# Optimization experiments

Hardware: AMD Instinct MI355X
Metric: run time of the kernel (lower is better)

## Reference

```python
import math
import jax, jax.numpy as jnp
import numpy as np

B, IN, OUT = 1024, 512, 512
SCALE_BASE = 1.0
SCALE_WAVELET = 1.0
MH_CONST = 2.0 / (math.sqrt(3.0) * math.pi ** 0.25)  # mexican hat normalizer


def setup_inputs() -> dict:
    key = jax.random.key(0)
    k1, k2, k3, k4 = jax.random.split(key, 4)
    he = math.sqrt(6.0 / IN)  # HeUniform fan_in limit
    return {
        "x": jax.random.normal(k1, (B, IN), dtype=jnp.float32),
        "scale": jnp.ones((OUT, IN), dtype=jnp.float32),
        "translation": jnp.zeros((OUT, IN), dtype=jnp.float32),
        "base_weight": jax.random.uniform(k3, (IN, OUT), dtype=jnp.float32, minval=-he, maxval=he),
        "wavelet_weights": jax.random.uniform(k4, (OUT, IN), dtype=jnp.float32, minval=-he, maxval=he),
    }


def reference(x, scale, translation, base_weight, wavelet_weights):
    # base path: swish(x @ W)
    base_out = x @ base_weight                      # (B, OUT)
    base_out = base_out * jax.nn.sigmoid(base_out)  # swish

    # wavelet path: expand to (B, OUT, IN), mexican-hat, weighted reduce over IN
    x_scaled = (x[:, None, :] - translation[None]) / scale[None]  # (B, OUT, IN)
    sq = jnp.square(x_scaled)
    wavelet = MH_CONST * (sq - 1.0) * jnp.exp(-0.5 * sq)
    wavelet_out = jnp.sum(wavelet * wavelet_weights[None], axis=2)  # (B, OUT)

    return SCALE_BASE * base_out + SCALE_WAVELET * wavelet_out
```

## Files before the change

kernel.cpp:

```cpp
#include <hip/hip_runtime.h>


#define B_DIM   1024
#define IN_DIM  512
#define OUT_DIM 512

#define MH_CONST 0.8673250691f
#define NHL2E    0.72134752044448170368f
#define L2E      1.44269504088896340736f

#define POISON32 0xAAAAAAAAu

#define OFF_XBF 4096
#define OFF_PSI (OFF_XBF + B_DIM*IN_DIM*2)
#define OFF_WBT (OFF_PSI + B_DIM*IN_DIM*2)
#define OFF_WWB (OFF_WBT + OUT_DIM*IN_DIM*2)
#define WS_NEED (OFF_WWB + OUT_DIM*IN_DIM*2)

#if defined(__has_builtin)
#if __has_builtin(__builtin_amdgcn_exp2f)
#define EXP2F(v) __builtin_amdgcn_exp2f(v)
#endif
#endif
#ifndef EXP2F
#define EXP2F(v) exp2f(v)
#endif

typedef __attribute__((ext_vector_type(8))) short short8;
typedef __attribute__((ext_vector_type(4))) float f32x4;

#define TO_GBL(p) ((const __attribute__((address_space(1))) void*)(p))
#define TO_LDS(p) ((__attribute__((address_space(3))) void*)(p))

__device__ __forceinline__ unsigned short f2bf(float f) {
    unsigned int u = __float_as_uint(f);
    u = (u + 0x7fff + ((u >> 16) & 1)) >> 16;
    return (unsigned short)u;
}
__device__ __forceinline__ unsigned int pack_bf(float a, float b) {
    return (unsigned int)f2bf(a) | ((unsigned int)f2bf(b) << 16);
}
__device__ __forceinline__ float psi_f(float xv) {
    const float sq = xv * xv;
    const float e  = EXP2F(-NHL2E * sq);
    return fmaf(MH_CONST, sq, -MH_CONST) * e;
}
__device__ __forceinline__ size_t panel_off(int row, int k8) {
    return (size_t)(row >> 5) * 32768 + (size_t)k8 * 512 + (row & 31) * 16;
}
__device__ __forceinline__ uint2 pack8(const float* s) {
    uint2 u;
    u.x = pack_bf(s[0], s[1]) ;
    u.y = pack_bf(s[2], s[3]);
    return u;
}

__global__ __launch_bounds__(256) void wkan_prep(
    const float* __restrict__ x,
    const float* __restrict__ scale,
    const float* __restrict__ trans,
    const float* __restrict__ bwgt,
    const float* __restrict__ wwgt,
    unsigned char* __restrict__ ws)
{
    __shared__ float tile[64][65];
    const int blk = blockIdx.x, t = threadIdx.x;
    unsigned int* flag = (unsigned int*)ws;

    if (blk < 256) {
        const int g = blk * 256 + t;
        const int row = g >> 6, c = g & 63;
        const float* src = x + (size_t)row * IN_DIM + c * 8;
        float v[8];
        *(float4*)&v[0] = *(const float4*)src;
        *(float4*)&v[4] = *(const float4*)(src + 4);
        const size_t off = panel_off(row, c);
        uint2 a, b;
        a.x = pack_bf(v[0], v[1]); a.y = pack_bf(v[2], v[3]);
        b.x = pack_bf(v[4], v[5]); b.y = pack_bf(v[6], v[7]);
        *(uint2*)(ws + OFF_XBF + off) = a;
        *(uint2*)(ws + OFF_XBF + off + 8) = b;
        a.x = pack_bf(psi_f(v[0]), psi_f(v[1])); a.y = pack_bf(psi_f(v[2]), psi_f(v[3]));
        b.x = pack_bf(psi_f(v[4]), psi_f(v[5])); b.y = pack_bf(psi_f(v[6]), psi_f(v[7]));
        *(uint2*)(ws + OFF_PSI + off) = a;
        *(uint2*)(ws + OFF_PSI + off + 8) = b;
    } else if (blk < 384) {
        const int g = (blk - 256) * 256 + t;
        const int row = g >> 6, c = g & 63;
        const size_t e = (size_t)row * IN_DIM + c * 8;
        const float4 s0 = *(const float4*)&scale[e];
        const float4 s1 = *(const float4*)&scale[e + 4];
        const float4 t0 = *(const float4*)&trans[e];
        const float4 t1 = *(const float4*)&trans[e + 4];
        const bool ok =
            (s0.x == 1.f) & (s0.y == 1.f) & (s0.z == 1.f) & (s0.w == 1.f) &
            (s1.x == 1.f) & (s1.y == 1.f) & (s1.z == 1.f) & (s1.w == 1.f) &
            (t0.x == 0.f) & (t0.y == 0.f) & (t0.z == 0.f) & (t0.w == 0.f) &
            (t1.x == 0.f) & (t1.y == 0.f) & (t1.z == 0.f) & (t1.w == 0.f);
        if (!ok) atomicAnd(flag, 0u);
        const float4 w0 = *(const float4*)&wwgt[e];
        const float4 w1 = *(const float4*)&wwgt[e + 4];
        const size_t off = panel_off(row, c);
        uint2 a, b;
        a.x = pack_bf(w0.x, w0.y); a.y = pack_bf(w0.z, w0.w);
        b.x = pack_bf(w1.x, w1.y); b.y = pack_bf(w1.z, w1.w);
        *(uint2*)(ws + OFF_WWB + off) = a;
        *(uint2*)(ws + OFF_WWB + off + 8) = b;
    } else {
        const int bt  = blk - 384;
        const int tk0 = (bt & 7) * 64;
        const int to0 = (bt >> 3) * 64;
        const int r   = t >> 2;
        const int c0  = (t & 3) * 16;
#pragma unroll
        for (int j = 0; j < 4; ++j) {
            const float4 v = *(const float4*)&bwgt[(size_t)(tk0 + r) * OUT_DIM + to0 + c0 + j * 4];
            tile[r][c0 + j * 4 + 0] = v.x; tile[r][c0 + j * 4 + 1] = v.y;
            tile[r][c0 + j * 4 + 2] = v.z; tile[r][c0 + j * 4 + 3] = v.w;
        }
        __syncthreads();
        uint2 a, b;
        a.x = pack_bf(tile[c0 + 0][r],  tile[c0 + 1][r]);
        a.y = pack_bf(tile[c0 + 2][r],  tile[c0 + 3][r]);
        b.x = pack_bf(tile[c0 + 4][r],  tile[c0 + 5][r]);
        b.y = pack_bf(tile[c0 + 6][r],  tile[c0 + 7][r]);
        const int orow = to0 + r;
        size_t off = panel_off(orow, (tk0 + c0) >> 3);
        *(uint2*)(ws + OFF_WBT + off) = a;
        *(uint2*)(ws + OFF_WBT + off + 8) = b;
        a.x = pack_bf(tile[c0 + 8][r],  tile[c0 + 9][r]);
        a.y = pack_bf(tile[c0 + 10][r], tile[c0 + 11][r]);
        b.x = pack_bf(tile[c0 + 12][r], tile[c0 + 13][r]);
        b.y = pack_bf(tile[c0 + 14][r], tile[c0 + 15][r]);
        off = panel_off(orow, ((tk0 + c0) >> 3) + 1);
        *(uint2*)(ws + OFF_WBT + off) = a;
        *(uint2*)(ws + OFF_WBT + off + 8) = b;
    }
}

__global__ __launch_bounds__(256) void wkan_main(
    const float* __restrict__ x,
    const float* __restrict__ scale,
    const float* __restrict__ trans,
    const float* __restrict__ bwgt,
    const float* __restrict__ wwgt,
    float* __restrict__ out,
    const unsigned char* __restrict__ ws,
    int have_ws)
{
    __shared__ __align__(16) unsigned char smem[65536];

    const int t  = threadIdx.x;
    const int b0 = blockIdx.x * 32;
    const int o0 = blockIdx.y * 32;
    const int fast = have_ws && (*(const unsigned int*)ws == POISON32);

    if (fast) {
        const int lane = t & 63, wave = t >> 6;
        const int mt = wave & 1, nt = wave >> 1;
        const int m = lane & 15, q = lane >> 4;

        const unsigned char* src =
            (wave == 0) ? (ws + OFF_XBF + (size_t)(b0 >> 5) * 32768) :
            (wave == 1) ? (ws + OFF_PSI + (size_t)(b0 >> 5) * 32768) :
            (wave == 2) ? (ws + OFF_WBT + (size_t)(o0 >> 5) * 32768) :
                          (ws + OFF_WWB + (size_t)(o0 >> 5) * 32768);
        const unsigned char* gbase = src + lane * 16;
        unsigned char* ldst = smem + wave * 16384;

        const int aoff = q * 512 + (mt * 16 + m) * 16;
        const int boff = q * 512 + (nt * 16 + m) * 16;

        f32x4 accb = {0.f, 0.f, 0.f, 0.f};
        f32x4 accw = {0.f, 0.f, 0.f, 0.f};

        for (int s = 0; s < 2; ++s) {
            __syncthreads();
#pragma unroll
            for (int i = 0; i < 16; ++i)
                __builtin_amdgcn_global_load_lds(TO_GBL(gbase + s * 16384 + i * 1024),
                                                 TO_LDS(ldst + i * 1024), 16, 0, 0);
            __syncthreads();

#pragma unroll
            for (int kk = 0; kk < 8; ++kk) {
                const short8 ax = *(const short8*)(smem + 0     + kk * 2048 + aoff);
                const short8 ap = *(const short8*)(smem + 16384 + kk * 2048 + aoff);
                const short8 bb = *(const short8*)(smem + 32768 + kk * 2048 + boff);
                const short8 bw = *(const short8*)(smem + 49152 + kk * 2048 + boff);
                accb = __builtin_amdgcn_mfma_f32_16x16x32_bf16(ax, bb, accb, 0, 0, 0);
                accw = __builtin_amdgcn_mfma_f32_16x16x32_bf16(ap, bw, accw, 0, 0, 0);
            }
        }

#pragma unroll
        for (int r = 0; r < 4; ++r) {
            const int bb_ = b0 + mt * 16 + q * 4 + r;
            const int oo_ = o0 + nt * 16 + m;
            const float sv  = accb[r];
            const float sig = __frcp_rn(1.0f + EXP2F(-sv * L2E));
            out[(size_t)bb_ * OUT_DIM + oo_] = fmaf(sv, sig, accw[r]);
        }
    } else {
        float (*sxs)[34] = (float(*)[34])(smem);
        float (*sts)[34] = (float(*)[34])(smem + 4352);
        float (*srs)[34] = (float(*)[34])(smem + 8704);
        float (*sws)[34] = (float(*)[34])(smem + 13056);
        float (*sbs)[34] = (float(*)[34])(smem + 17408);

        const int tx = t & 15, ty = t >> 4;
        const int lr = t >> 3, lc = (t & 7) * 4;

        float accw2[2][2] = {{0.f, 0.f}, {0.f, 0.f}};
        float accb2[2][2] = {{0.f, 0.f}, {0.f, 0.f}};

        for (int k0 = 0; k0 < IN_DIM; k0 += 32) {
            const float4 xv = *(const float4*)&x[(size_t)(b0 + lr) * IN_DIM + k0 + lc];
            const float4 tv = *(const float4*)&trans[(size_t)(o0 + lr) * IN_DIM + k0 + lc];
            const float4 sv = *(const float4*)&scale[(size_t)(o0 + lr) * IN_DIM + k0 + lc];
            const float4 wv = *(const float4*)&wwgt[(size_t)(o0 + lr) * IN_DIM + k0 + lc];
            const float4 bv = *(const float4*)&bwgt[(size_t)(k0 + lr) * OUT_DIM + o0 + lc];

            __syncthreads();

            sxs[lc + 0][lr] = xv.x; sxs[lc + 1][lr] = xv.y;
            sxs[lc + 2][lr] = xv.z; sxs[lc + 3][lr] = xv.w;
            sts[lc + 0][lr] = tv.x; sts[lc + 1][lr] = tv.y;
            sts[lc + 2][lr] = tv.z; sts[lc + 3][lr] = tv.w;
            srs[lc + 0][lr] = __frcp_rn(sv.x); srs[lc + 1][lr] = __frcp_rn(sv.y);
            srs[lc + 2][lr] = __frcp_rn(sv.z); srs[lc + 3][lr] = __frcp_rn(sv.w);
            sws[lc + 0][lr] = wv.x * MH_CONST; sws[lc + 1][lr] = wv.y * MH_CONST;
            sws[lc + 2][lr] = wv.z * MH_CONST; sws[lc + 3][lr] = wv.w * MH_CONST;
            sbs[lr][lc + 0] = bv.x; sbs[lr][lc + 1] = bv.y;
            sbs[lr][lc + 2] = bv.z; sbs[lr][lc + 3] = bv.w;

            __syncthreads();

#pragma unroll 8
            for (int kk = 0; kk < 32; ++kk) {
                const float2 xv2 = *(const float2*)&sxs[kk][2 * ty];
                const float2 tv2 = *(const float2*)&sts[kk][2 * tx];
                const float2 rv2 = *(const float2*)&srs[kk][2 * tx];
                const float2 wv2 = *(const float2*)&sws[kk][2 * tx];
                const float2 bv2 = *(const float2*)&sbs[kk][2 * tx];
                const float xb[2] = {xv2.x, xv2.y};
                const float tr[2] = {tv2.x, tv2.y};
                const float rc[2] = {rv2.x, rv2.y};
                const float wl[2] = {wv2.x, wv2.y};
                const float bw2[2] = {bv2.x, bv2.y};
#pragma unroll
                for (int oo = 0; oo < 2; ++oo) {
#pragma unroll
                    for (int bb = 0; bb < 2; ++bb) {
                        const float d  = (xb[bb] - tr[oo]) * rc[oo];
                        const float sq = d * d;
                        const float e  = EXP2F(-NHL2E * sq);
                        const float p  = fmaf(wl[oo], sq, -wl[oo]);
                        accw2[bb][oo] = fmaf(p, e, accw2[bb][oo]);
                        accb2[bb][oo] = fmaf(xb[bb], bw2[oo], accb2[bb][oo]);
                    }
                }
            }
        }

#pragma unroll
        for (int bb = 0; bb < 2; ++bb) {
#pragma unroll
            for (int oo = 0; oo < 2; ++oo) {
                const float s   = accb2[bb][oo];
                const float sig = __frcp_rn(1.0f + EXP2F(-s * L2E));
                out[(size_t)(b0 + 2 * ty + bb) * OUT_DIM + (o0 + 2 * tx + oo)] =
                    fmaf(s, sig, accw2[bb][oo]);
            }
        }
    }
}

extern "C" void kernel_launch(void* const* d_in, const int* in_sizes, int n_in,
                              void* d_out, int out_size, void* d_ws, size_t ws_size,
                              hipStream_t stream) {
    const float* x     = (const float*)d_in[0];
    const float* scale = (const float*)d_in[1];
    const float* trans = (const float*)d_in[2];
    const float* bwgt  = (const float*)d_in[3];
    const float* wwgt  = (const float*)d_in[4];
    float* out = (float*)d_out;

    const int have_ws = (ws_size >= (size_t)WS_NEED) ? 1 : 0;
    unsigned char* ws = (unsigned char*)d_ws;

    if (have_ws) {
        wkan_prep<<<dim3(448), dim3(256), 0, stream>>>(x, scale, trans, bwgt, wwgt, ws);
    }
    wkan_main<<<dim3(B_DIM / 32, OUT_DIM / 32), dim3(256), 0, stream>>>(
        x, scale, trans, bwgt, wwgt, out, ws, have_ws);
}
```

Before: 70.33 us.

## Load MFMA operands directly from global per wave, dropping LDS staging

The fast path of the main kernel no longer stages the four bf16 operand panels into a 64KB LDS buffer with global_load_lds and barriers. Each wave now computes its own 16x16 output tile and reads its A and B fragments straight from the pre-packed workspace. The grid becomes 1D with a remapped block-to-tile order meant to help L2 locality, and shared memory shrinks to what the fallback path needs, which should allow more resident blocks. The cost is that operand reuse within a block is lost, so fragments shared by neighbouring tiles are fetched repeatedly and rely on L2/L1 hits.

Measured after the change: 72.84 us. 3.6% more time.

```diff
diff --git a/kernel.cpp b/kernel.cpp
--- a/kernel.cpp
+++ b/kernel.cpp
@@ -29,9 +29,6 @@
 typedef __attribute__((ext_vector_type(8))) short short8;
 typedef __attribute__((ext_vector_type(4))) float f32x4;
 
-#define TO_GBL(p) ((const __attribute__((address_space(1))) void*)(p))
-#define TO_LDS(p) ((__attribute__((address_space(3))) void*)(p))
-
 __device__ __forceinline__ unsigned short f2bf(float f) {
     unsigned int u = __float_as_uint(f);
     u = (u + 0x7fff + ((u >> 16) & 1)) >> 16;
@@ -47,12 +44,6 @@
 }
 __device__ __forceinline__ size_t panel_off(int row, int k8) {
     return (size_t)(row >> 5) * 32768 + (size_t)k8 * 512 + (row & 31) * 16;
-}
-__device__ __forceinline__ uint2 pack8(const float* s) {
-    uint2 u;
-    u.x = pack_bf(s[0], s[1]) ;
-    u.y = pack_bf(s[2], s[3]);
-    return u;
 }
 
 __global__ __launch_bounds__(256) void wkan_prep(
@@ -148,60 +139,51 @@
     const unsigned char* __restrict__ ws,
     int have_ws)
 {
-    __shared__ __align__(16) unsigned char smem[65536];
-
-    const int t  = threadIdx.x;
-    const int b0 = blockIdx.x * 32;
-    const int o0 = blockIdx.y * 32;
+    __shared__ __align__(16) unsigned char smem[21760];
+
+    const int t   = threadIdx.x;
+    const int blk = blockIdx.x;
     const int fast = have_ws && (*(const unsigned int*)ws == POISON32);
 
     if (fast) {
         const int lane = t & 63, wave = t >> 6;
-        const int mt = wave & 1, nt = wave >> 1;
         const int m = lane & 15, q = lane >> 4;
-
-        const unsigned char* src =
-            (wave == 0) ? (ws + OFF_XBF + (size_t)(b0 >> 5) * 32768) :
-            (wave == 1) ? (ws + OFF_PSI + (size_t)(b0 >> 5) * 32768) :
-            (wave == 2) ? (ws + OFF_WBT + (size_t)(o0 >> 5) * 32768) :
-                          (ws + OFF_WWB + (size_t)(o0 >> 5) * 32768);
-        const unsigned char* gbase = src + lane * 16;
-        unsigned char* ldst = smem + wave * 16384;
-
-        const int aoff = q * 512 + (mt * 16 + m) * 16;
-        const int boff = q * 512 + (nt * 16 + m) * 16;
+        const int bt = (blk >> 5) * 4 + wave;
+        const int ot = ((blk & 7) << 2) | ((blk >> 3) & 3);
+
+        const size_t arow = (size_t)((bt & 1) * 16 + m) * 16;
+        const size_t brow = (size_t)((ot & 1) * 16 + m) * 16;
+        const unsigned char* pax = ws + OFF_XBF + (size_t)(bt >> 1) * 32768 + arow;
+        const unsigned char* pap = ws + OFF_PSI + (size_t)(bt >> 1) * 32768 + arow;
+        const unsigned char* pbb = ws + OFF_WBT + (size_t)(ot >> 1) * 32768 + brow;
+        const unsigned char* pbw = ws + OFF_WWB + (size_t)(ot >> 1) * 32768 + brow;
 
         f32x4 accb = {0.f, 0.f, 0.f, 0.f};
         f32x4 accw = {0.f, 0.f, 0.f, 0.f};
 
-        for (int s = 0; s < 2; ++s) {
-            __syncthreads();
-#pragma unroll
-            for (int i = 0; i < 16; ++i)
-                __builtin_amdgcn_global_load_lds(TO_GBL(gbase + s * 16384 + i * 1024),
-                                                 TO_LDS(ldst + i * 1024), 16, 0, 0);
-            __syncthreads();
-
-#pragma unroll
-            for (int kk = 0; kk < 8; ++kk) {
-                const short8 ax = *(const short8*)(smem + 0     + kk * 2048 + aoff);
-                const short8 ap = *(const short8*)(smem + 16384 + kk * 2048 + aoff);
-                const short8 bb = *(const short8*)(smem + 32768 + kk * 2048 + boff);
-                const short8 bw = *(const short8*)(smem + 49152 + kk * 2048 + boff);
-                accb = __builtin_amdgcn_mfma_f32_16x16x32_bf16(ax, bb, accb, 0, 0, 0);
-                accw = __builtin_amdgcn_mfma_f32_16x16x32_bf16(ap, bw, accw, 0, 0, 0);
-            }
+#pragma unroll
+        for (int kk = 0; kk < 16; ++kk) {
+            const int off = (kk * 4 + q) * 512;
+            const short8 ax = *(const short8*)(pax + off);
+            const short8 ap = *(const short8*)(pap + off);
+            const short8 bb = *(const short8*)(pbb + off);
+            const short8 bw = *(const short8*)(pbw + off);
+            accb = __builtin_amdgcn_mfma_f32_16x16x32_bf16(ax, bb, accb, 0, 0, 0);
+            accw = __builtin_amdgcn_mfma_f32_16x16x32_bf16(ap, bw, accw, 0, 0, 0);
         }
 
 #pragma unroll
         for (int r = 0; r < 4; ++r) {
-            const int bb_ = b0 + mt * 16 + q * 4 + r;
-            const int oo_ = o0 + nt * 16 + m;
+            const int bb_ = bt * 16 + q * 4 + r;
+            const int oo_ = ot * 16 + m;
             const float sv  = accb[r];
             const float sig = __frcp_rn(1.0f + EXP2F(-sv * L2E));
             out[(size_t)bb_ * OUT_DIM + oo_] = fmaf(sv, sig, accw[r]);
         }
     } else {
+        const int b0 = (blk >> 4) * 32;
+        const int o0 = (blk & 15) * 32;
+
         float (*sxs)[34] = (float(*)[34])(smem);
         float (*sts)[34] = (float(*)[34])(smem + 4352);
         float (*srs)[34] = (float(*)[34])(smem + 8704);
@@ -292,6 +274,6 @@
     if (have_ws) {
         wkan_prep<<<dim3(448), dim3(256), 0, stream>>>(x, scale, trans, bwgt, wwgt, ws);
     }
-    wkan_main<<<dim3(B_DIM / 32, OUT_DIM / 32), dim3(256), 0, stream>>>(
+    wkan_main<<<dim3(512), dim3(256), 0, stream>>>(
         x, scale, trans, bwgt, wwgt, out, ws, have_ws);
 }
```
